# Optimization experiments

Hardware: AMD Instinct MI355X
Metric: run time of the kernel (lower is better)

## Reference

```python
import jax, jax.numpy as jnp
import numpy as np

B, L, D, NH, NV, T = 4096, 5, 128, 16, 4, 100
NUM_USERS = NUM_ITEMS = 100000
FC1_DIM = NV * D + NH * sum(L - l + 1 for l in range(1, L + 1))  # 752


def setup_inputs() -> dict:
    key = jax.random.key(0)
    ks = jax.random.split(key, 12)
    s = 0.02
    return {
        "seq": jax.random.randint(ks[0], (B, L), 0, NUM_ITEMS),
        "user": jax.random.randint(ks[1], (B,), 0, NUM_USERS),
        "items": jax.random.randint(ks[2], (B, T), 0, NUM_ITEMS),
        "item_table": jax.random.normal(ks[3], (NUM_ITEMS, D), jnp.float32) * s,
        "user_table": jax.random.normal(ks[4], (NUM_USERS, D), jnp.float32) * s,
        "Wv": jax.random.normal(ks[5], (NV, L), jnp.float32) * s,
        "bv": jnp.zeros((NV,), jnp.float32),
        "Wh": jax.random.normal(ks[6], (L, NH, L, D), jnp.float32) * s,
        "bh": jnp.zeros((L, NH), jnp.float32),
        "W1": jax.random.normal(ks[7], (FC1_DIM, D), jnp.float32) * s,
        "b1": jnp.zeros((D,), jnp.float32),
        "W2_table": jax.random.normal(ks[8], (NUM_ITEMS, 2 * D), jnp.float32) * s,
        "b2_table": jnp.zeros((NUM_ITEMS, 1), jnp.float32),
        "_predict": 1,
    }


def reference(seq, user, items, item_table, user_table, Wv, bv, Wh, bh, W1, b1, W2_table, b2_table, _predict):
    emb = item_table[seq]            # (B, L, D)
    uemb = user_table[user]          # (B, D)

    # vertical conv: kernel (L,1), nv out channels -> (B, NV, D), flattened
    ver = jnp.einsum("btd,vt->bvd", emb, Wv) + bv[None, :, None]
    ver_flat = ver.reshape(B, NV * D)

    # horizontal convs: for each kernel length l, NH filters of shape (l, D)
    hor = []
    for l in range(1, L + 1):
        lout = L - l + 1
        # windows: (B, lout, l, D) built from l shifted views
        win = jnp.stack([emb[:, s:s + lout] for s in range(l)], axis=2)
        h = jnp.einsum("btsd,fsd->bft", win, Wh[l - 1, :, :l]) + bh[l - 1][None, :, None]
        hor.append(jax.nn.relu(h).reshape(B, NH * lout))

    z = jnp.concatenate([ver_flat] + hor, axis=1)      # (B, FC1_DIM)
    x = jax.nn.relu(z @ W1 + b1)                        # (B, D)
    xc = jnp.concatenate([x, uemb], axis=1)             # (B, 2D)

    w2 = W2_table[items]                                # (B, T, 2D)
    b2 = b2_table[items][..., 0]                        # (B, T)
    res = jnp.einsum("btd,bd->bt", w2, xc) + b2
    return res
```

## Files before the change

### kernel.cpp

```cpp
#include <hip/hip_runtime.h>


constexpr int Bsz  = 4096;
constexpr int Lq   = 5;
constexpr int Dd   = 128;
constexpr int EP   = 132;
constexpr int NHh  = 16;
constexpr int NVv  = 4;
constexpr int Tt   = 100;
constexpr int FC1  = 752;
constexpr int KQ   = FC1 / 4;
constexpr int G    = 4;
constexpr int NTHR = 256;

__global__ __launch_bounds__(NTHR, 4) void caser_front(
    const int* __restrict__ seq, const int* __restrict__ user,
    const float* __restrict__ item_table, const float* __restrict__ user_table,
    const float* __restrict__ Wv, const float* __restrict__ bv,
    const float* __restrict__ Wh, const float* __restrict__ bh,
    const float* __restrict__ W1, const float* __restrict__ b1,
    float* __restrict__ xc_ws)
{
    __shared__ float emb[G][Lq * EP];
    __shared__ float z[G][FC1];
    __shared__ float xc[G][2 * Dd];

    const int tid = threadIdx.x;
    const int b0  = blockIdx.x * G;
    float* embf = &emb[0][0];

    for (int idx = tid; idx < G * Lq * Dd; idx += NTHR) {
        int gt  = idx >> 7;
        int d   = idx & (Dd - 1);
        int row = seq[b0 * Lq + gt];
        embf[gt * EP + d] = item_table[row * Dd + d];
    }
    for (int idx = tid; idx < G * Dd; idx += NTHR) {
        int g = idx >> 7, d = idx & (Dd - 1);
        xc[g][Dd + d] = user_table[user[b0 + g] * Dd + d];
    }
    __syncthreads();

    for (int idx = tid; idx < G * NVv * Dd; idx += NTHR) {
        int g = idx >> 9;
        int v = (idx >> 7) & 3;
        int d = idx & (Dd - 1);
        float acc = bv[v];
        #pragma unroll
        for (int t = 0; t < Lq; ++t)
            acc = fmaf(emb[g][t * EP + d], Wv[v * Lq + t], acc);
        z[g][v * Dd + d] = acc;
    }

    if (tid < 240) {
        int glt = tid >> 4, f = tid & 15;
        int l, t;
        if      (glt < 5)  { l = 1; t = glt; }
        else if (glt < 9)  { l = 2; t = glt - 5; }
        else if (glt < 12) { l = 3; t = glt - 9; }
        else if (glt < 14) { l = 4; t = glt - 12; }
        else               { l = 5; t = 0; }
        const int lout = Lq - l + 1;
        const int zoff = (l == 1) ? 0 : (l == 2) ? 80 : (l == 3) ? 144
                       : (l == 4) ? 192 : 224;
        float acc[G];
        {
            float bias = bh[(l - 1) * NHh + f];
            #pragma unroll
            for (int g = 0; g < G; ++g) acc[g] = bias;
        }
        const float4* w4 = reinterpret_cast<const float4*>(
            Wh + (((l - 1) * NHh + f) * Lq) * Dd);
        float4 wc = w4[t == t ? 0 : 0];
        wc = w4[0];
        const int niter = l * 32;
        for (int it = 0; it < niter; ++it) {
            float4 wn = (it + 1 < niter) ? w4[it + 1] : wc;
            const int s  = it >> 5;
            const int d4 = it & 31;
            const int ebase = (t + s) * EP + d4 * 4;
            #pragma unroll
            for (int g = 0; g < G; ++g) {
                float4 e = *reinterpret_cast<const float4*>(
                    &embf[g * Lq * EP + ebase]);
                acc[g] = fmaf(e.x, wc.x,
                         fmaf(e.y, wc.y,
                         fmaf(e.z, wc.z,
                         fmaf(e.w, wc.w, acc[g]))));
            }
            wc = wn;
        }
        #pragma unroll
        for (int g = 0; g < G; ++g)
            z[g][NVv * Dd + zoff + f * lout + t] = fmaxf(acc[g], 0.0f);
    }
    __syncthreads();

    float* part = &embf[0];
    {
        const int q  = tid >> 6;
        const int j2 = tid & 63;
        const float* w1p = W1 + 2 * j2;
        float2 acc[G];
        #pragma unroll
        for (int g = 0; g < G; ++g) acc[g] = make_float2(0.f, 0.f);
        const int i0 = q * KQ;
        float2 cw0, cw1, cw2, cw3, nw0, nw1, nw2, nw3;
        cw0 = *reinterpret_cast<const float2*>(w1p + (i0 + 0) * Dd);
        cw1 = *reinterpret_cast<const float2*>(w1p + (i0 + 1) * Dd);
        cw2 = *reinterpret_cast<const float2*>(w1p + (i0 + 2) * Dd);
        cw3 = *reinterpret_cast<const float2*>(w1p + (i0 + 3) * Dd);
        for (int i = i0; i < i0 + KQ - 4; i += 4) {
            nw0 = *reinterpret_cast<const float2*>(w1p + (i + 4) * Dd);
            nw1 = *reinterpret_cast<const float2*>(w1p + (i + 5) * Dd);
            nw2 = *reinterpret_cast<const float2*>(w1p + (i + 6) * Dd);
            nw3 = *reinterpret_cast<const float2*>(w1p + (i + 7) * Dd);
            #pragma unroll
            for (int g = 0; g < G; ++g) {
                float4 zz = *reinterpret_cast<const float4*>(&z[g][i]);
                acc[g].x = fmaf(zz.w, cw3.x, fmaf(zz.z, cw2.x,
                           fmaf(zz.y, cw1.x, fmaf(zz.x, cw0.x, acc[g].x))));
                acc[g].y = fmaf(zz.w, cw3.y, fmaf(zz.z, cw2.y,
                           fmaf(zz.y, cw1.y, fmaf(zz.x, cw0.y, acc[g].y))));
            }
            cw0 = nw0; cw1 = nw1; cw2 = nw2; cw3 = nw3;
        }
        {
            const int i = i0 + KQ - 4;
            #pragma unroll
            for (int g = 0; g < G; ++g) {
                float4 zz = *reinterpret_cast<const float4*>(&z[g][i]);
                acc[g].x = fmaf(zz.w, cw3.x, fmaf(zz.z, cw2.x,
                           fmaf(zz.y, cw1.x, fmaf(zz.x, cw0.x, acc[g].x))));
                acc[g].y = fmaf(zz.w, cw3.y, fmaf(zz.z, cw2.y,
                           fmaf(zz.y, cw1.y, fmaf(zz.x, cw0.y, acc[g].y))));
            }
        }
        #pragma unroll
        for (int g = 0; g < G; ++g)
            *reinterpret_cast<float2*>(&part[(q * G + g) * Dd + 2 * j2])
                = acc[g];
    }
    __syncthreads();
    if (tid < Dd) {
        #pragma unroll
        for (int g = 0; g < G; ++g) {
            float s = part[g * Dd + tid]
                    + part[(G + g) * Dd + tid]
                    + part[(2 * G + g) * Dd + tid]
                    + part[(3 * G + g) * Dd + tid];
            xc[g][tid] = fmaxf(s + b1[tid], 0.0f);
        }
    }
    __syncthreads();

    for (int idx = tid; idx < G * 2 * Dd; idx += NTHR)
        xc_ws[b0 * 2 * Dd + idx] = xc[0][idx];
}

__global__ __launch_bounds__(NTHR, 6) void caser_tail(
    const int* __restrict__ items,
    const float* __restrict__ W2_table, const float* __restrict__ b2_table,
    const float* __restrict__ xc_ws, float* __restrict__ out)
{
    __shared__ int   s_items[Tt];
    __shared__ float s_b2[Tt];

    const int b    = blockIdx.x;
    const int tid  = threadIdx.x;
    const int lane = tid & 63;
    const int wv   = tid >> 6;

    if (tid < Tt) {
        int it = items[b * Tt + tid];
        s_items[tid] = it;
        s_b2[tid]    = b2_table[it];
    }
    const float4 xf =
        reinterpret_cast<const float4*>(xc_ws + b * 2 * Dd)[lane];
    __syncthreads();

    #pragma unroll 5
    for (int k = 0; k < Tt / 4; ++k) {
        const int t = wv + k * 4;
        const float4* wp = reinterpret_cast<const float4*>(
            W2_table + (size_t)s_items[t] * (2 * Dd));
        float4 w = wp[lane];
        float v = fmaf(w.x, xf.x,
                  fmaf(w.y, xf.y,
                  fmaf(w.z, xf.z, w.w * xf.w)));
        #pragma unroll
        for (int off = 32; off; off >>= 1)
            v += __shfl_xor(v, off);
        if (lane == 0) out[b * Tt + t] = v + s_b2[t];
    }
}

extern "C" void kernel_launch(void* const* d_in, const int* in_sizes, int n_in,
                              void* d_out, int out_size, void* d_ws, size_t ws_size,
                              hipStream_t stream) {
    const int*   seq        = (const int*)  d_in[0];
    const int*   user       = (const int*)  d_in[1];
    const int*   items      = (const int*)  d_in[2];
    const float* item_table = (const float*)d_in[3];
    const float* user_table = (const float*)d_in[4];
    const float* Wv         = (const float*)d_in[5];
    const float* bv         = (const float*)d_in[6];
    const float* Wh         = (const float*)d_in[7];
    const float* bh         = (const float*)d_in[8];
    const float* W1         = (const float*)d_in[9];
    const float* b1         = (const float*)d_in[10];
    const float* W2_table   = (const float*)d_in[11];
    const float* b2_table   = (const float*)d_in[12];
    float* out   = (float*)d_out;
    float* xc_ws = (float*)d_ws;

    caser_front<<<dim3(Bsz / G), dim3(NTHR), 0, stream>>>(
        seq, user, item_table, user_table, Wv, bv, Wh, bh, W1, b1, xc_ws);
    caser_tail<<<dim3(Bsz), dim3(NTHR), 0, stream>>>(
        items, W2_table, b2_table, xc_ws, out);
}
```

Baseline: 327.1 us.

## Widen front kernel to 512 threads and restructure tail gather to 16-lane groups

The front kernel doubles its block size to 512 threads. Horizontal-conv work is split across two half-warps per filter, combined with a shuffle, and assigned to waves in a rotated order via a packed lookup code. The FC1 GEMV now gives each thread one output column instead of two. The tail kernel has each 16-lane group handle one item row with four float4 loads per lane plus a prefetch of the next row, cutting the shuffle reduction to four steps. The aim is more parallelism and memory-level concurrency in both kernels, at the cost of higher register pressure and a 512-thread block that may lower occupancy.

```diff
diff --git a/kernel.cpp b/kernel.cpp
--- a/kernel.cpp
+++ b/kernel.cpp
@@ -9,11 +9,17 @@
 constexpr int NVv  = 4;
 constexpr int Tt   = 100;
 constexpr int FC1  = 752;
-constexpr int KQ   = FC1 / 4;
 constexpr int G    = 4;
-constexpr int NTHR = 256;
-
-__global__ __launch_bounds__(NTHR, 4) void caser_front(
+constexpr int NTA  = 512;
+constexpr int NTB  = 256;
+
+__device__ __forceinline__ unsigned p2b_code(int eglt) {
+    const unsigned long long lo = 0x2230214120401050ULL;
+    const unsigned long long hi = 0x0014131211322331ULL;
+    return (unsigned)(((eglt & 8) ? hi : lo) >> ((eglt & 7) * 8)) & 0xffu;
+}
+
+__global__ __launch_bounds__(NTA, 4) void caser_front(
     const int* __restrict__ seq, const int* __restrict__ user,
     const float* __restrict__ item_table, const float* __restrict__ user_table,
     const float* __restrict__ Wv, const float* __restrict__ bv,
@@ -25,23 +31,25 @@
     __shared__ float z[G][FC1];
     __shared__ float xc[G][2 * Dd];
 
-    const int tid = threadIdx.x;
-    const int b0  = blockIdx.x * G;
+    const int tid  = threadIdx.x;
+    const int lane = tid & 63;
+    const int wv   = tid >> 6;
+    const int b0   = blockIdx.x * G;
     float* embf = &emb[0][0];
 
-    for (int idx = tid; idx < G * Lq * Dd; idx += NTHR) {
+    for (int idx = tid; idx < G * Lq * Dd; idx += NTA) {
         int gt  = idx >> 7;
         int d   = idx & (Dd - 1);
         int row = seq[b0 * Lq + gt];
         embf[gt * EP + d] = item_table[row * Dd + d];
     }
-    for (int idx = tid; idx < G * Dd; idx += NTHR) {
+    for (int idx = tid; idx < G * Dd; idx += NTA) {
         int g = idx >> 7, d = idx & (Dd - 1);
         xc[g][Dd + d] = user_table[user[b0 + g] * Dd + d];
     }
     __syncthreads();
 
-    for (int idx = tid; idx < G * NVv * Dd; idx += NTHR) {
+    for (int idx = tid; idx < G * NVv * Dd; idx += NTA) {
         int g = idx >> 9;
         int v = (idx >> 7) & 3;
         int d = idx & (Dd - 1);
@@ -52,101 +60,100 @@
         z[g][v * Dd + d] = acc;
     }
 
-    if (tid < 240) {
-        int glt = tid >> 4, f = tid & 15;
-        int l, t;
-        if      (glt < 5)  { l = 1; t = glt; }
-        else if (glt < 9)  { l = 2; t = glt - 5; }
-        else if (glt < 12) { l = 3; t = glt - 9; }
-        else if (glt < 14) { l = 4; t = glt - 12; }
-        else               { l = 5; t = 0; }
-        const int lout = Lq - l + 1;
-        const int zoff = (l == 1) ? 0 : (l == 2) ? 80 : (l == 3) ? 144
-                       : (l == 4) ? 192 : 224;
-        float acc[G];
-        {
-            float bias = bh[(l - 1) * NHh + f];
+    {
+        const int ewv  = (wv + (int)blockIdx.x) & 7;
+        const int eglt = ewv * 2 + (lane >> 5);
+        const unsigned code = p2b_code(eglt);
+        if (code) {
+            const int l    = code >> 4;
+            const int t    = code & 15;
+            const int half = (lane >> 4) & 1;
+            const int f    = lane & 15;
+            const int lout = Lq - l + 1;
+            const int zoff = (l == 1) ? 0 : (l == 2) ? 80 : (l == 3) ? 144
+                           : (l == 4) ? 192 : 224;
+            const int dbase = half * 64;
+            float acc[G] = {0.f, 0.f, 0.f, 0.f};
+            const float* whb = Wh + (((l - 1) * NHh + f) * Lq) * Dd + dbase;
+            const int niter = l * 16;
+            float4 wc = *reinterpret_cast<const float4*>(whb);
+            for (int it = 0; it < niter; ++it) {
+                const int nx = it + 1;
+                float4 wn = (nx < niter)
+                    ? *reinterpret_cast<const float4*>(
+                          whb + (nx >> 4) * Dd + (nx & 15) * 4)
+                    : wc;
+                const int s  = it >> 4;
+                const int d4 = it & 15;
+                const int eb = (t + s) * EP + dbase + d4 * 4;
+                #pragma unroll
+                for (int g = 0; g < G; ++g) {
+                    float4 e = *reinterpret_cast<const float4*>(
+                        &embf[g * Lq * EP + eb]);
+                    acc[g] = fmaf(e.x, wc.x,
+                             fmaf(e.y, wc.y,
+                             fmaf(e.z, wc.z,
+                             fmaf(e.w, wc.w, acc[g]))));
+                }
+                wc = wn;
+            }
             #pragma unroll
-            for (int g = 0; g < G; ++g) acc[g] = bias;
-        }
-        const float4* w4 = reinterpret_cast<const float4*>(
-            Wh + (((l - 1) * NHh + f) * Lq) * Dd);
-        float4 wc = w4[t == t ? 0 : 0];
-        wc = w4[0];
-        const int niter = l * 32;
-        for (int it = 0; it < niter; ++it) {
-            float4 wn = (it + 1 < niter) ? w4[it + 1] : wc;
-            const int s  = it >> 5;
-            const int d4 = it & 31;
-            const int ebase = (t + s) * EP + d4 * 4;
-            #pragma unroll
-            for (int g = 0; g < G; ++g) {
-                float4 e = *reinterpret_cast<const float4*>(
-                    &embf[g * Lq * EP + ebase]);
-                acc[g] = fmaf(e.x, wc.x,
-                         fmaf(e.y, wc.y,
-                         fmaf(e.z, wc.z,
-                         fmaf(e.w, wc.w, acc[g]))));
-            }
-            wc = wn;
-        }
-        #pragma unroll
-        for (int g = 0; g < G; ++g)
-            z[g][NVv * Dd + zoff + f * lout + t] = fmaxf(acc[g], 0.0f);
+            for (int g = 0; g < G; ++g)
+                acc[g] += __shfl_xor(acc[g], 16);
+            if (!half) {
+                const float bias = bh[(l - 1) * NHh + f];
+                #pragma unroll
+                for (int g = 0; g < G; ++g)
+                    z[g][NVv * Dd + zoff + f * lout + t]
+                        = fmaxf(acc[g] + bias, 0.0f);
+            }
+        }
     }
     __syncthreads();
 
     float* part = &embf[0];
     {
-        const int q  = tid >> 6;
-        const int j2 = tid & 63;
-        const float* w1p = W1 + 2 * j2;
-        float2 acc[G];
-        #pragma unroll
-        for (int g = 0; g < G; ++g) acc[g] = make_float2(0.f, 0.f);
-        const int i0 = q * KQ;
-        float2 cw0, cw1, cw2, cw3, nw0, nw1, nw2, nw3;
-        cw0 = *reinterpret_cast<const float2*>(w1p + (i0 + 0) * Dd);
-        cw1 = *reinterpret_cast<const float2*>(w1p + (i0 + 1) * Dd);
-        cw2 = *reinterpret_cast<const float2*>(w1p + (i0 + 2) * Dd);
-        cw3 = *reinterpret_cast<const float2*>(w1p + (i0 + 3) * Dd);
-        for (int i = i0; i < i0 + KQ - 4; i += 4) {
-            nw0 = *reinterpret_cast<const float2*>(w1p + (i + 4) * Dd);
-            nw1 = *reinterpret_cast<const float2*>(w1p + (i + 5) * Dd);
-            nw2 = *reinterpret_cast<const float2*>(w1p + (i + 6) * Dd);
-            nw3 = *reinterpret_cast<const float2*>(w1p + (i + 7) * Dd);
+        const int q = tid >> 7;
+        const int j = tid & 127;
+        const float* w1p = W1 + j;
+        float acc[G] = {0.f, 0.f, 0.f, 0.f};
+        const int i0 = q * 188;
+        float c0 = w1p[(i0 + 0) * Dd];
+        float c1 = w1p[(i0 + 1) * Dd];
+        float c2 = w1p[(i0 + 2) * Dd];
+        float c3 = w1p[(i0 + 3) * Dd];
+        for (int i = i0; i < i0 + 188 - 4; i += 4) {
+            float n0 = w1p[(i + 4) * Dd];
+            float n1 = w1p[(i + 5) * Dd];
+            float n2 = w1p[(i + 6) * Dd];
+            float n3 = w1p[(i + 7) * Dd];
             #pragma unroll
             for (int g = 0; g < G; ++g) {
                 float4 zz = *reinterpret_cast<const float4*>(&z[g][i]);
-                acc[g].x = fmaf(zz.w, cw3.x, fmaf(zz.z, cw2.x,
-                           fmaf(zz.y, cw1.x, fmaf(zz.x, cw0.x, acc[g].x))));
-                acc[g].y = fmaf(zz.w, cw3.y, fmaf(zz.z, cw2.y,
-                           fmaf(zz.y, cw1.y, fmaf(zz.x, cw0.y, acc[g].y))));
-            }
-            cw0 = nw0; cw1 = nw1; cw2 = nw2; cw3 = nw3;
+                acc[g] = fmaf(zz.x, c0, fmaf(zz.y, c1,
+                         fmaf(zz.z, c2, fmaf(zz.w, c3, acc[g]))));
+            }
+            c0 = n0; c1 = n1; c2 = n2; c3 = n3;
         }
         {
-            const int i = i0 + KQ - 4;
+            const int i = i0 + 188 - 4;
             #pragma unroll
             for (int g = 0; g < G; ++g) {
                 float4 zz = *reinterpret_cast<const float4*>(&z[g][i]);
-                acc[g].x = fmaf(zz.w, cw3.x, fmaf(zz.z, cw2.x,
-                           fmaf(zz.y, cw1.x, fmaf(zz.x, cw0.x, acc[g].x))));
-                acc[g].y = fmaf(zz.w, cw3.y, fmaf(zz.z, cw2.y,
-                           fmaf(zz.y, cw1.y, fmaf(zz.x, cw0.y, acc[g].y))));
+                acc[g] = fmaf(zz.x, c0, fmaf(zz.y, c1,
+                         fmaf(zz.z, c2, fmaf(zz.w, c3, acc[g]))));
             }
         }
         #pragma unroll
         for (int g = 0; g < G; ++g)
-            *reinterpret_cast<float2*>(&part[(q * G + g) * Dd + 2 * j2])
-                = acc[g];
+            part[(q * G + g) * Dd + j] = acc[g];
     }
     __syncthreads();
     if (tid < Dd) {
         #pragma unroll
         for (int g = 0; g < G; ++g) {
-            float s = part[g * Dd + tid]
-                    + part[(G + g) * Dd + tid]
+            float s = part[(0 * G + g) * Dd + tid]
+                    + part[(1 * G + g) * Dd + tid]
                     + part[(2 * G + g) * Dd + tid]
                     + part[(3 * G + g) * Dd + tid];
             xc[g][tid] = fmaxf(s + b1[tid], 0.0f);
@@ -154,11 +161,11 @@
     }
     __syncthreads();
 
-    for (int idx = tid; idx < G * 2 * Dd; idx += NTHR)
+    for (int idx = tid; idx < G * 2 * Dd; idx += NTA)
         xc_ws[b0 * 2 * Dd + idx] = xc[0][idx];
 }
 
-__global__ __launch_bounds__(NTHR, 6) void caser_tail(
+__global__ __launch_bounds__(NTB, 6) void caser_tail(
     const int* __restrict__ items,
     const float* __restrict__ W2_table, const float* __restrict__ b2_table,
     const float* __restrict__ xc_ws, float* __restrict__ out)
@@ -170,29 +177,70 @@
     const int tid  = threadIdx.x;
     const int lane = tid & 63;
     const int wv   = tid >> 6;
+    const int grp  = lane >> 4;
+    const int sub  = lane & 15;
+    const int gidx = wv * 4 + grp;
 
     if (tid < Tt) {
         int it = items[b * Tt + tid];
         s_items[tid] = it;
         s_b2[tid]    = b2_table[it];
     }
-    const float4 xf =
-        reinterpret_cast<const float4*>(xc_ws + b * 2 * Dd)[lane];
-    __syncthreads();
-
-    #pragma unroll 5
-    for (int k = 0; k < Tt / 4; ++k) {
-        const int t = wv + k * 4;
+    const float4* xcp = reinterpret_cast<const float4*>(
+        xc_ws + b * 2 * Dd + sub * 16);
+    const float4 x0 = xcp[0], x1 = xcp[1], x2 = xcp[2], x3 = xcp[3];
+    __syncthreads();
+
+    float4 c0, c1, c2, c3;
+    {
         const float4* wp = reinterpret_cast<const float4*>(
-            W2_table + (size_t)s_items[t] * (2 * Dd));
-        float4 w = wp[lane];
-        float v = fmaf(w.x, xf.x,
-                  fmaf(w.y, xf.y,
-                  fmaf(w.z, xf.z, w.w * xf.w)));
-        #pragma unroll
-        for (int off = 32; off; off >>= 1)
-            v += __shfl_xor(v, off);
-        if (lane == 0) out[b * Tt + t] = v + s_b2[t];
+            W2_table + (size_t)s_items[gidx] * (2 * Dd) + sub * 16);
+        c0 = wp[0]; c1 = wp[1]; c2 = wp[2]; c3 = wp[3];
+    }
+    for (int r = 0; r < 6; ++r) {
+        float4 n0, n1, n2, n3;
+        if (r < 5) {
+            const float4* wp = reinterpret_cast<const float4*>(
+                W2_table + (size_t)s_items[(r + 1) * 16 + gidx] * (2 * Dd)
+                + sub * 16);
+            n0 = wp[0]; n1 = wp[1]; n2 = wp[2]; n3 = wp[3];
+        }
+        const int t = r * 16 + gidx;
+        float p0 = fmaf(c0.x, x0.x, fmaf(c0.y, x0.y,
+                   fmaf(c0.z, x0.z, c0.w * x0.w)));
+        float p1 = fmaf(c1.x, x1.x, fmaf(c1.y, x1.y,
+                   fmaf(c1.z, x1.z, c1.w * x1.w)));
+        float p2 = fmaf(c2.x, x2.x, fmaf(c2.y, x2.y,
+                   fmaf(c2.z, x2.z, c2.w * x2.w)));
+        float p3 = fmaf(c3.x, x3.x, fmaf(c3.y, x3.y,
+                   fmaf(c3.z, x3.z, c3.w * x3.w)));
+        float v = (p0 + p1) + (p2 + p3);
+        v += __shfl_xor(v, 1);
+        v += __shfl_xor(v, 2);
+        v += __shfl_xor(v, 4);
+        v += __shfl_xor(v, 8);
+        if (sub == 0) out[b * Tt + t] = v + s_b2[t];
+        if (r < 5) { c0 = n0; c1 = n1; c2 = n2; c3 = n3; }
+    }
+    if (gidx < 4) {
+        const int t = 96 + gidx;
+        const float4* wp = reinterpret_cast<const float4*>(
+            W2_table + (size_t)s_items[t] * (2 * Dd) + sub * 16);
+        float4 w0 = wp[0], w1 = wp[1], w2 = wp[2], w3 = wp[3];
+        float p0 = fmaf(w0.x, x0.x, fmaf(w0.y, x0.y,
+                   fmaf(w0.z, x0.z, w0.w * x0.w)));
+        float p1 = fmaf(w1.x, x1.x, fmaf(w1.y, x1.y,
+                   fmaf(w1.z, x1.z, w1.w * x1.w)));
+        float p2 = fmaf(w2.x, x2.x, fmaf(w2.y, x2.y,
+                   fmaf(w2.z, x2.z, w2.w * x2.w)));
+        float p3 = fmaf(w3.x, x3.x, fmaf(w3.y, x3.y,
+                   fmaf(w3.z, x3.z, w3.w * x3.w)));
+        float v = (p0 + p1) + (p2 + p3);
+        v += __shfl_xor(v, 1);
+        v += __shfl_xor(v, 2);
+        v += __shfl_xor(v, 4);
+        v += __shfl_xor(v, 8);
+        if (sub == 0) out[b * Tt + t] = v + s_b2[t];
     }
 }
 
@@ -215,8 +263,8 @@
     float* out   = (float*)d_out;
     float* xc_ws = (float*)d_ws;
 
-    caser_front<<<dim3(Bsz / G), dim3(NTHR), 0, stream>>>(
+    caser_front<<<dim3(Bsz / G), dim3(NTA), 0, stream>>>(
         seq, user, item_table, user_table, Wv, bv, Wh, bh, W1, b1, xc_ws);
-    caser_tail<<<dim3(Bsz), dim3(NTHR), 0, stream>>>(
+    caser_tail<<<dim3(Bsz), dim3(NTB), 0, stream>>>(
         items, W2_table, b2_table, xc_ws, out);
 }
```

Result: slower. 363.9 us (+11.2%).

## Gather W2 rows with 16-lane groups and prefetch; halve front batch group

Applied to the files above, without the earlier changes.

The tail kernel now gives each W2 row to a 16-lane group instead of a full 64-lane wave. Each lane loads four float4 values, and the next row is prefetched while the current one is reduced. This needs fewer shuffle steps per output and keeps more gather loads in flight. The front kernel drops from 4 to 2 batch rows per block, which doubles the grid but also doubles W1 reads per batch row from L2. The horizontal-conv bias is now added after accumulation rather than used as the starting value.

```diff
diff --git a/kernel.cpp b/kernel.cpp
--- a/kernel.cpp
+++ b/kernel.cpp
@@ -10,8 +10,9 @@
 constexpr int Tt   = 100;
 constexpr int FC1  = 752;
 constexpr int KQ   = FC1 / 4;
-constexpr int G    = 4;
+constexpr int G    = 2;
 constexpr int NTHR = 256;
+constexpr int NTB  = 256;
 
 __global__ __launch_bounds__(NTHR, 4) void caser_front(
     const int* __restrict__ seq, const int* __restrict__ user,
@@ -63,17 +64,11 @@
         const int lout = Lq - l + 1;
         const int zoff = (l == 1) ? 0 : (l == 2) ? 80 : (l == 3) ? 144
                        : (l == 4) ? 192 : 224;
-        float acc[G];
-        {
-            float bias = bh[(l - 1) * NHh + f];
-            #pragma unroll
-            for (int g = 0; g < G; ++g) acc[g] = bias;
-        }
+        float acc[G] = {0.f, 0.f};
         const float4* w4 = reinterpret_cast<const float4*>(
             Wh + (((l - 1) * NHh + f) * Lq) * Dd);
-        float4 wc = w4[t == t ? 0 : 0];
-        wc = w4[0];
         const int niter = l * 32;
+        float4 wc = w4[0];
         for (int it = 0; it < niter; ++it) {
             float4 wn = (it + 1 < niter) ? w4[it + 1] : wc;
             const int s  = it >> 5;
@@ -90,9 +85,11 @@
             }
             wc = wn;
         }
+        const float bias = bh[(l - 1) * NHh + f];
         #pragma unroll
         for (int g = 0; g < G; ++g)
-            z[g][NVv * Dd + zoff + f * lout + t] = fmaxf(acc[g], 0.0f);
+            z[g][NVv * Dd + zoff + f * lout + t]
+                = fmaxf(acc[g] + bias, 0.0f);
     }
     __syncthreads();
 
@@ -105,16 +102,16 @@
         #pragma unroll
         for (int g = 0; g < G; ++g) acc[g] = make_float2(0.f, 0.f);
         const int i0 = q * KQ;
-        float2 cw0, cw1, cw2, cw3, nw0, nw1, nw2, nw3;
+        float2 cw0, cw1, cw2, cw3;
         cw0 = *reinterpret_cast<const float2*>(w1p + (i0 + 0) * Dd);
         cw1 = *reinterpret_cast<const float2*>(w1p + (i0 + 1) * Dd);
         cw2 = *reinterpret_cast<const float2*>(w1p + (i0 + 2) * Dd);
         cw3 = *reinterpret_cast<const float2*>(w1p + (i0 + 3) * Dd);
         for (int i = i0; i < i0 + KQ - 4; i += 4) {
-            nw0 = *reinterpret_cast<const float2*>(w1p + (i + 4) * Dd);
-            nw1 = *reinterpret_cast<const float2*>(w1p + (i + 5) * Dd);
-            nw2 = *reinterpret_cast<const float2*>(w1p + (i + 6) * Dd);
-            nw3 = *reinterpret_cast<const float2*>(w1p + (i + 7) * Dd);
+            float2 nw0 = *reinterpret_cast<const float2*>(w1p + (i + 4) * Dd);
+            float2 nw1 = *reinterpret_cast<const float2*>(w1p + (i + 5) * Dd);
+            float2 nw2 = *reinterpret_cast<const float2*>(w1p + (i + 6) * Dd);
+            float2 nw3 = *reinterpret_cast<const float2*>(w1p + (i + 7) * Dd);
             #pragma unroll
             for (int g = 0; g < G; ++g) {
                 float4 zz = *reinterpret_cast<const float4*>(&z[g][i]);
@@ -145,8 +142,8 @@
     if (tid < Dd) {
         #pragma unroll
         for (int g = 0; g < G; ++g) {
-            float s = part[g * Dd + tid]
-                    + part[(G + g) * Dd + tid]
+            float s = part[(0 * G + g) * Dd + tid]
+                    + part[(1 * G + g) * Dd + tid]
                     + part[(2 * G + g) * Dd + tid]
                     + part[(3 * G + g) * Dd + tid];
             xc[g][tid] = fmaxf(s + b1[tid], 0.0f);
@@ -158,7 +155,7 @@
         xc_ws[b0 * 2 * Dd + idx] = xc[0][idx];
 }
 
-__global__ __launch_bounds__(NTHR, 6) void caser_tail(
+__global__ __launch_bounds__(NTB, 6) void caser_tail(
     const int* __restrict__ items,
     const float* __restrict__ W2_table, const float* __restrict__ b2_table,
     const float* __restrict__ xc_ws, float* __restrict__ out)
@@ -170,29 +167,70 @@
     const int tid  = threadIdx.x;
     const int lane = tid & 63;
     const int wv   = tid >> 6;
+    const int grp  = lane >> 4;
+    const int sub  = lane & 15;
+    const int gidx = wv * 4 + grp;
 
     if (tid < Tt) {
         int it = items[b * Tt + tid];
         s_items[tid] = it;
         s_b2[tid]    = b2_table[it];
     }
-    const float4 xf =
-        reinterpret_cast<const float4*>(xc_ws + b * 2 * Dd)[lane];
-    __syncthreads();
-
-    #pragma unroll 5
-    for (int k = 0; k < Tt / 4; ++k) {
-        const int t = wv + k * 4;
+    const float4* xcp = reinterpret_cast<const float4*>(
+        xc_ws + b * 2 * Dd + sub * 16);
+    const float4 x0 = xcp[0], x1 = xcp[1], x2 = xcp[2], x3 = xcp[3];
+    __syncthreads();
+
+    float4 c0, c1, c2, c3;
+    {
         const float4* wp = reinterpret_cast<const float4*>(
-            W2_table + (size_t)s_items[t] * (2 * Dd));
-        float4 w = wp[lane];
-        float v = fmaf(w.x, xf.x,
-                  fmaf(w.y, xf.y,
-                  fmaf(w.z, xf.z, w.w * xf.w)));
-        #pragma unroll
-        for (int off = 32; off; off >>= 1)
-            v += __shfl_xor(v, off);
-        if (lane == 0) out[b * Tt + t] = v + s_b2[t];
+            W2_table + (size_t)s_items[gidx] * (2 * Dd) + sub * 16);
+        c0 = wp[0]; c1 = wp[1]; c2 = wp[2]; c3 = wp[3];
+    }
+    for (int r = 0; r < 6; ++r) {
+        float4 n0, n1, n2, n3;
+        if (r < 5) {
+            const float4* wp = reinterpret_cast<const float4*>(
+                W2_table + (size_t)s_items[(r + 1) * 16 + gidx] * (2 * Dd)
+                + sub * 16);
+            n0 = wp[0]; n1 = wp[1]; n2 = wp[2]; n3 = wp[3];
+        }
+        const int t = r * 16 + gidx;
+        float p0 = fmaf(c0.x, x0.x, fmaf(c0.y, x0.y,
+                   fmaf(c0.z, x0.z, c0.w * x0.w)));
+        float p1 = fmaf(c1.x, x1.x, fmaf(c1.y, x1.y,
+                   fmaf(c1.z, x1.z, c1.w * x1.w)));
+        float p2 = fmaf(c2.x, x2.x, fmaf(c2.y, x2.y,
+                   fmaf(c2.z, x2.z, c2.w * x2.w)));
+        float p3 = fmaf(c3.x, x3.x, fmaf(c3.y, x3.y,
+                   fmaf(c3.z, x3.z, c3.w * x3.w)));
+        float v = (p0 + p1) + (p2 + p3);
+        v += __shfl_xor(v, 1);
+        v += __shfl_xor(v, 2);
+        v += __shfl_xor(v, 4);
+        v += __shfl_xor(v, 8);
+        if (sub == 0) out[b * Tt + t] = v + s_b2[t];
+        if (r < 5) { c0 = n0; c1 = n1; c2 = n2; c3 = n3; }
+    }
+    if (gidx < 4) {
+        const int t = 96 + gidx;
+        const float4* wp = reinterpret_cast<const float4*>(
+            W2_table + (size_t)s_items[t] * (2 * Dd) + sub * 16);
+        float4 w0 = wp[0], w1 = wp[1], w2 = wp[2], w3 = wp[3];
+        float p0 = fmaf(w0.x, x0.x, fmaf(w0.y, x0.y,
+                   fmaf(w0.z, x0.z, w0.w * x0.w)));
+        float p1 = fmaf(w1.x, x1.x, fmaf(w1.y, x1.y,
+                   fmaf(w1.z, x1.z, w1.w * x1.w)));
+        float p2 = fmaf(w2.x, x2.x, fmaf(w2.y, x2.y,
+                   fmaf(w2.z, x2.z, w2.w * x2.w)));
+        float p3 = fmaf(w3.x, x3.x, fmaf(w3.y, x3.y,
+                   fmaf(w3.z, x3.z, w3.w * x3.w)));
+        float v = (p0 + p1) + (p2 + p3);
+        v += __shfl_xor(v, 1);
+        v += __shfl_xor(v, 2);
+        v += __shfl_xor(v, 4);
+        v += __shfl_xor(v, 8);
+        if (sub == 0) out[b * Tt + t] = v + s_b2[t];
     }
 }
 
@@ -217,6 +255,6 @@
 
     caser_front<<<dim3(Bsz / G), dim3(NTHR), 0, stream>>>(
         seq, user, item_table, user_table, Wv, bv, Wh, bh, W1, b1, xc_ws);
-    caser_tail<<<dim3(Bsz), dim3(NTHR), 0, stream>>>(
+    caser_tail<<<dim3(Bsz), dim3(NTB), 0, stream>>>(
         items, W2_table, b2_table, xc_ws, out);
 }
```

Measured after the change: 379.8 us. +16.1%, slower.
